# Kernel optimization log

Measured on AMD Instinct MI355X. Metric: run time of the kernel, lower is better.

The kernel has to match this reference:

```python
import jax, jax.numpy as jnp
import numpy as np

B, DIN, DOUT, E, H, K = 8192, 1024, 1024, 8, 128, 2

def setup_inputs() -> dict:
    key = jax.random.key(0)
    ks = jax.random.split(key, 6)
    s = 0.02
    return {
        "x": jax.random.normal(ks[0], (B, DIN), jnp.float32),
        "w1": jax.random.normal(ks[1], (DIN, H), jnp.float32) * s,
        "b1": jnp.zeros((H,), jnp.float32),
        "wg": jax.random.normal(ks[2], (DIN, H), jnp.float32) * s,
        "bg": jnp.zeros((H,), jnp.float32),
        "w2": jax.random.normal(ks[3], (H, E), jnp.float32) * s,
        "b2": jnp.zeros((E,), jnp.float32),
        "we": jax.random.normal(ks[4], (E, DIN, DOUT), jnp.float32) * s,
        "be": jnp.zeros((E, DOUT), jnp.float32),
    }

def reference(x, w1, b1, wg, bg, w2, b2, we, be):
    Bx = x.shape[0]
    Eo = we.shape[0]
    Do = we.shape[2]
    # Router with GLU; NOTE: softmax over BATCH dim (dim=0), as in source.
    h = (x @ w1 + b1) * jax.nn.relu(x @ wg + bg)
    h = jax.nn.relu(h)
    l = jax.nn.softmax(x=(h @ w2 + b2), axis=0)  # [B, E]
    batch_K = -(-K * Bx) // Eo  # ceil(K/E * B), static
    # top-k tokens per expert (along batch dim)
    ws_t, ib_t = jax.lax.top_k(l.T, batch_K)  # [E, bK]
    ws, ib = ws_t.T, ib_t.T                   # [bK, E]
    nws = jax.nn.softmax(ws, axis=0)          # renorm over selected tokens
    # dispatch: gather selected tokens for all experts at once
    sel = x[ib]                                # [bK, E, DIN]
    eo = jnp.einsum('ked,edo->keo', sel, we) + be  # [bK, E, DOUT]
    eo = eo * nws[:, :, None]
    # combine (concat_sum): per-expert scatter-set + shared scatter-add sum
    e_idx = jnp.broadcast_to(jnp.arange(Eo)[None, :], ib.shape)  # [bK, E]
    out_e = jnp.zeros((Eo, Bx, Do), x.dtype).at[e_idx, ib].set(eo)
    temp_sum = jnp.zeros((Bx, Do), x.dtype).at[ib].add(eo)
    out_e = out_e + temp_sum[None]
    return out_e.transpose(1, 0, 2).reshape(Bx, Eo * Do)
```

## Files before the change

kernel.cpp:

```cpp
#include <hip/hip_runtime.h>
#include <math.h>

#define B_TOK 8192
#define D_IN 1024
#define D_OUT 1024
#define N_E 8
#define N_H 128
#define SEL 2048

using bf16x8 = __attribute__((ext_vector_type(8))) short;
using floatx4 = __attribute__((ext_vector_type(4))) float;

__device__ __forceinline__ unsigned short f2bf(float f) {
  unsigned u = __float_as_uint(f);
  u = (u + 0x7FFFu + ((u >> 16) & 1u)) >> 16;
  return (unsigned short)u;
}

__device__ __forceinline__ float bf2f(unsigned short h) {
  return __uint_as_float(((unsigned)h) << 16);
}

__device__ __forceinline__ void async_cp16(const void* g, void* l) {
  __builtin_amdgcn_global_load_lds((__attribute__((address_space(1))) void*)g,
                                   (__attribute__((address_space(3))) void*)l,
                                   16, 0, 0);
}

__global__ __launch_bounds__(256) void k_router_fat(const float* __restrict__ x,
                                                    const float* __restrict__ w1,
                                                    const float* __restrict__ b1,
                                                    const float* __restrict__ wg,
                                                    const float* __restrict__ bg,
                                                    const float* __restrict__ w2,
                                                    const float* __restrict__ b2,
                                                    const float* __restrict__ we,
                                                    unsigned short* __restrict__ xb,
                                                    double* __restrict__ logits,
                                                    unsigned short* __restrict__ web) {
  __shared__ char smem[39168];
  const int t = threadIdx.x;

  if (blockIdx.x >= 512) {
    const int wb = blockIdx.x - 512;
    const int e = wb >> 8;
    const int rem = wb & 255;
    const int o0 = (rem >> 4) * 64;
    const int d0 = (rem & 15) * 64;
    float (*tile)[68] = (float(*)[68])smem;
    const float* wsrc = we + (size_t)e * D_IN * D_OUT;
    unsigned short* wdst = web + (size_t)e * D_OUT * D_IN;
    const int r = t >> 4;
    const int c = (t & 15) * 4;
#pragma unroll
    for (int p = 0; p < 4; ++p) {
      float4 v = *(const float4*)(wsrc + (size_t)(d0 + r + 16 * p) * D_OUT + o0 + c);
      tile[r + 16 * p][c] = v.x; tile[r + 16 * p][c + 1] = v.y;
      tile[r + 16 * p][c + 2] = v.z; tile[r + 16 * p][c + 3] = v.w;
    }
    __syncthreads();
#pragma unroll
    for (int p = 0; p < 4; ++p) {
      int orow = r + 16 * p;
      ushort4 v;
      v.x = f2bf(tile[c + 0][orow]); v.y = f2bf(tile[c + 1][orow]);
      v.z = f2bf(tile[c + 2][orow]); v.w = f2bf(tile[c + 3][orow]);
      *(ushort4*)(wdst + (size_t)(o0 + orow) * D_IN + d0 + c) = v;
    }
    return;
  }

  float (*xs)[36]  = (float(*)[36])(smem);
  float (*ws1)[128] = (float(*)[128])(smem + 2304);
  float (*wsg)[128] = (float(*)[128])(smem + 2304 + 16384);
  float* w2s = (float*)(smem + 2304 + 16384 + 16384);
  const int b0 = blockIdx.x * 16;
  const int tg = t >> 5;
  const int og = t & 31;

  ((float4*)w2s)[t] = ((const float4*)w2)[t];

  double d1[2][4] = {}; double dg[2][4] = {};
  for (int k0 = 0; k0 < D_IN; k0 += 32) {
    __syncthreads();
    if (t < 128) {
      int r = t >> 3, c = (t & 7) * 4;
      float4 v = *(const float4*)(x + (size_t)(b0 + r) * D_IN + k0 + c);
      *(float4*)(&xs[r][c]) = v;
      ushort4 u; u.x = f2bf(v.x); u.y = f2bf(v.y); u.z = f2bf(v.z); u.w = f2bf(v.w);
      *(ushort4*)(xb + (size_t)(b0 + r) * D_IN + k0 + c) = u;
    }
    {
      int r = t >> 5, c = (t & 31) * 4;
#pragma unroll
      for (int p = 0; p < 4; ++p) {
        *(float4*)(&ws1[r + 8 * p][c]) = *(const float4*)(w1 + (size_t)(k0 + r + 8 * p) * N_H + c);
        *(float4*)(&wsg[r + 8 * p][c]) = *(const float4*)(wg + (size_t)(k0 + r + 8 * p) * N_H + c);
      }
    }
    __syncthreads();
    float a1[2][4] = {}; float ag[2][4] = {};
    for (int k = 0; k < 32; k += 4) {
      float xk[2][4];
#pragma unroll
      for (int i = 0; i < 2; ++i) {
        float4 v = *(const float4*)(&xs[tg * 2 + i][k]);
        xk[i][0] = v.x; xk[i][1] = v.y; xk[i][2] = v.z; xk[i][3] = v.w;
      }
#pragma unroll
      for (int kk = 0; kk < 4; ++kk) {
        float4 w1v = *(const float4*)(&ws1[k + kk][og * 4]);
        float4 wgv = *(const float4*)(&wsg[k + kk][og * 4]);
        float wa1[4] = {w1v.x, w1v.y, w1v.z, w1v.w};
        float wag[4] = {wgv.x, wgv.y, wgv.z, wgv.w};
#pragma unroll
        for (int i = 0; i < 2; ++i) {
#pragma unroll
          for (int j = 0; j < 4; ++j) {
            a1[i][j] += xk[i][kk] * wa1[j];
            ag[i][j] += xk[i][kk] * wag[j];
          }
        }
      }
    }
#pragma unroll
    for (int i = 0; i < 2; ++i)
#pragma unroll
      for (int j = 0; j < 4; ++j) { d1[i][j] += a1[i][j]; dg[i][j] += ag[i][j]; }
  }

  float4 b1v = *(const float4*)(b1 + og * 4);
  float4 bgv = *(const float4*)(bg + og * 4);
  float b1a[4] = {b1v.x, b1v.y, b1v.z, b1v.w};
  float bga[4] = {bgv.x, bgv.y, bgv.z, bgv.w};
  float hv[2][4];
#pragma unroll
  for (int i = 0; i < 2; ++i) {
#pragma unroll
    for (int j = 0; j < 4; ++j) {
      float a = (float)d1[i][j] + b1a[j];
      float g = (float)dg[i][j] + bga[j];
      g = fmaxf(g, 0.f);
      hv[i][j] = fmaxf(a * g, 0.f);
    }
  }

  double lp[2][8] = {};
#pragma unroll
  for (int i = 0; i < 2; ++i) {
#pragma unroll
    for (int j = 0; j < 4; ++j) {
      double hj = (double)hv[i][j];
      int kk = og * 4 + j;
#pragma unroll
      for (int e = 0; e < 8; ++e)
        lp[i][e] += hj * (double)w2s[kk * N_E + e];
    }
  }
#pragma unroll
  for (int o = 16; o; o >>= 1) {
#pragma unroll
    for (int i = 0; i < 2; ++i)
#pragma unroll
      for (int e = 0; e < 8; ++e)
        lp[i][e] += __shfl_down(lp[i][e], o);
  }
  if (og == 0) {
#pragma unroll
    for (int i = 0; i < 2; ++i)
#pragma unroll
      for (int e = 0; e < 8; ++e)
        logits[(size_t)(b0 + tg * 2 + i) * N_E + e] = lp[i][e] + (double)b2[e];
  }
}

__global__ __launch_bounds__(256) void k_topk(const double* __restrict__ logits,
                                              int* __restrict__ ib, float* __restrict__ nws,
                                              int* __restrict__ slot) {
  const int e = blockIdx.x;
  const int t = threadIdx.x;
  __shared__ double redd[4];
  __shared__ int redi[4];
  __shared__ unsigned redu[4];
  __shared__ int s_cnt;

  double lv[32];
#pragma unroll
  for (int i = 0; i < 32; ++i) lv[i] = logits[(size_t)(t + i * 256) * N_E + e];

  double m = -1e300;
#pragma unroll
  for (int i = 0; i < 32; ++i) m = fmax(m, lv[i]);
  for (int o = 32; o; o >>= 1) m = fmax(m, __shfl_down(m, o));
  __syncthreads();
  if ((t & 63) == 0) redd[t >> 6] = m;
  __syncthreads();
  const double maxl = fmax(fmax(redd[0], redd[1]), fmax(redd[2], redd[3]));

  double s = 0.0;
#pragma unroll
  for (int i = 0; i < 32; ++i) s += exp(lv[i] - maxl);
  for (int o = 32; o; o >>= 1) s += __shfl_down(s, o);
  __syncthreads();
  if ((t & 63) == 0) redd[t >> 6] = s;
  __syncthreads();
  const double sum = redd[0] + redd[1] + redd[2] + redd[3];

  unsigned kr[32];
#pragma unroll
  for (int i = 0; i < 32; ++i) {
    float lf = (float)(exp(lv[i] - maxl) / sum);
    kr[i] = __float_as_uint(lf);
  }

  unsigned mnk = 0xFFFFFFFFu, mxk = 0;
#pragma unroll
  for (int i = 0; i < 32; ++i) { mnk = (kr[i] < mnk) ? kr[i] : mnk; mxk = (kr[i] > mxk) ? kr[i] : mxk; }
  for (int o = 32; o; o >>= 1) {
    unsigned v = __shfl_down(mnk, o); mnk = (v < mnk) ? v : mnk;
    unsigned w = __shfl_down(mxk, o); mxk = (w > mxk) ? w : mxk;
  }
  __syncthreads();
  if ((t & 63) == 0) redu[t >> 6] = mnk;
  __syncthreads();
  mnk = redu[0]; if (redu[1] < mnk) mnk = redu[1]; if (redu[2] < mnk) mnk = redu[2]; if (redu[3] < mnk) mnk = redu[3];
  __syncthreads();
  if ((t & 63) == 0) redu[t >> 6] = mxk;
  __syncthreads();
  mxk = redu[0]; if (redu[1] > mxk) mxk = redu[1]; if (redu[2] > mxk) mxk = redu[2]; if (redu[3] > mxk) mxk = redu[3];

  const unsigned diff = mnk ^ mxk;
  int hb = -1;
  unsigned thr;
  if (diff == 0) {
    thr = mnk;
  } else {
    hb = 31 - __clz(diff);
    thr = mxk & ~((hb >= 31) ? 0xFFFFFFFFu : ((1u << (hb + 1)) - 1u));
  }

  for (int bit = hb; bit >= 0; --bit) {
    unsigned trial = thr | (1u << bit);
    int c = 0;
#pragma unroll
    for (int i = 0; i < 32; ++i) c += (kr[i] >= trial) ? 1 : 0;
    for (int o = 32; o; o >>= 1) c += __shfl_down(c, o);
    __syncthreads();
    if ((t & 63) == 0) redi[t >> 6] = c;
    __syncthreads();
    c = redi[0] + redi[1] + redi[2] + redi[3];
    if (c >= SEL) thr = trial;
  }

  int c1 = 0, ceq = 0;
#pragma unroll
  for (int i = 0; i < 32; ++i) {
    c1 += (kr[i] > thr) ? 1 : 0;
    ceq += (kr[i] == thr) ? 1 : 0;
  }
  for (int o = 32; o; o >>= 1) { c1 += __shfl_down(c1, o); ceq += __shfl_down(ceq, o); }
  __syncthreads();
  if ((t & 63) == 0) { redi[t >> 6] = c1; ((int*)redu)[t >> 6] = ceq; }
  __syncthreads();
  c1 = redi[0] + redi[1] + redi[2] + redi[3];
  ceq = ((int*)redu)[0] + ((int*)redu)[1] + ((int*)redu)[2] + ((int*)redu)[3];
  const int need = SEL - c1;

  int cut;
  if (ceq == need) {
    cut = B_TOK;
  } else {
    cut = 0;
    for (int bit = 12; bit >= 0; --bit) {
      int trial = cut | (1 << bit);
      int c = 0;
#pragma unroll
      for (int i = 0; i < 32; ++i) c += (kr[i] == thr && (t + i * 256) < trial) ? 1 : 0;
      for (int o = 32; o; o >>= 1) c += __shfl_down(c, o);
      __syncthreads();
      if ((t & 63) == 0) redi[t >> 6] = c;
      __syncthreads();
      c = redi[0] + redi[1] + redi[2] + redi[3];
      if (c < need) cut = trial;
    }
  }

  const double maxw = (double)__uint_as_float(mxk);

  double ss = 0.0;
#pragma unroll
  for (int i = 0; i < 32; ++i) {
    int idx = t + i * 256;
    bool sel = (kr[i] > thr) || (kr[i] == thr && idx <= cut);
    if (sel) ss += exp((double)__uint_as_float(kr[i]) - maxw);
  }
  for (int o = 32; o; o >>= 1) ss += __shfl_down(ss, o);
  __syncthreads();
  if ((t & 63) == 0) redd[t >> 6] = ss;
  __syncthreads();
  const double ssum = redd[0] + redd[1] + redd[2] + redd[3];

  if (t == 0) s_cnt = 0;
#pragma unroll
  for (int i = 0; i < 32; ++i) slot[(size_t)(t + i * 256) * N_E + e] = -1;
  __syncthreads();
  for (int i = 0; i < 32; ++i) {
    int idx = t + i * 256;
    bool sel = (kr[i] > thr) || (kr[i] == thr && idx <= cut);
    if (sel) {
      int pos = atomicAdd(&s_cnt, 1);
      ib[e * SEL + pos] = idx;
      nws[e * SEL + pos] = (float)(exp((double)__uint_as_float(kr[i]) - maxw) / ssum);
      slot[(size_t)idx * N_E + e] = pos;
    }
  }
}

__global__ __launch_bounds__(512, 2) void k_expert_gemm(const unsigned short* __restrict__ xb,
                                                        const unsigned short* __restrict__ web,
                                                        const float* __restrict__ be,
                                                        const int* __restrict__ ib,
                                                        const float* __restrict__ nws,
                                                        unsigned short* __restrict__ eo) {
  __shared__ unsigned short S[2 * 32768];
  __shared__ int rowidx[256];
  __shared__ float nwss[256];
  const int e = blockIdx.z;
  const int bm = blockIdx.x * 256;
  const int bn = blockIdx.y * 256;
  const int t = threadIdx.x;
  const int wave = t >> 6, lane = t & 63;
  if (t < 256) {
    rowidx[t] = ib[e * SEL + bm + t];
    nwss[t] = nws[e * SEL + bm + t];
  }
  __syncthreads();
  const unsigned short* wbase = web + (size_t)e * D_IN * D_OUT;

  const unsigned short* asrc[4];
  const unsigned short* bsrc[4];
  int adst[4], bdst[4];
#pragma unroll
  for (int j = 0; j < 4; ++j) {
    int idx = t + j * 512;
    int r = idx >> 3;
    int c16 = (idx & 7) ^ (r & 7);
    asrc[j] = xb + (size_t)rowidx[r] * D_IN + c16 * 8;
    adst[j] = idx * 8;
    bsrc[j] = wbase + (size_t)(bn + r) * D_IN + c16 * 8;
    bdst[j] = 16384 + idx * 8;
  }

#define STAGE(kt, buf)                                                        \
  {                                                                           \
    _Pragma("unroll")                                                         \
    for (int j = 0; j < 4; ++j) {                                             \
      async_cp16(asrc[j] + (kt) * 64, S + (buf) * 32768 + adst[j]);           \
      async_cp16(bsrc[j] + (kt) * 64, S + (buf) * 32768 + bdst[j]);           \
    }                                                                         \
  }

  floatx4 acc[8][4] = {};
  const int wr = wave >> 2, wc = wave & 3;
  const int fr = lane & 15, fq = lane >> 4;
  const int swz = (fr & 7) << 3;

  STAGE(0, 0);
  STAGE(1, 1);

  for (int kt = 0; kt < 16; ++kt) {
    const int cur = kt & 1;
    if (kt == 15) {
      asm volatile("s_waitcnt vmcnt(0)" ::: "memory");
    } else {
      asm volatile("s_waitcnt vmcnt(8)" ::: "memory");
    }
    __builtin_amdgcn_s_barrier();
    const unsigned short* Ab = S + cur * 32768;
    const unsigned short* Bb = Ab + 16384;
    __builtin_amdgcn_s_setprio(1);
#pragma unroll
    for (int kk = 0; kk < 2; ++kk) {
      bf16x8 af[8], bfr[4];
#pragma unroll
      for (int mt = 0; mt < 8; ++mt)
        af[mt] = *(const bf16x8*)(Ab + (wr * 128 + mt * 16 + fr) * 64 + ((kk * 32 + fq * 8) ^ swz));
#pragma unroll
      for (int nt = 0; nt < 4; ++nt)
        bfr[nt] = *(const bf16x8*)(Bb + (wc * 64 + nt * 16 + fr) * 64 + ((kk * 32 + fq * 8) ^ swz));
#pragma unroll
      for (int mt = 0; mt < 8; ++mt)
#pragma unroll
        for (int nt = 0; nt < 4; ++nt)
          acc[mt][nt] = __builtin_amdgcn_mfma_f32_16x16x32_bf16(af[mt], bfr[nt], acc[mt][nt], 0, 0, 0);
    }
    __builtin_amdgcn_s_setprio(0);
    __builtin_amdgcn_sched_barrier(0);
    __builtin_amdgcn_s_barrier();
    if (kt < 14) STAGE(kt + 2, cur);
  }
#undef STAGE

  float bev[4];
#pragma unroll
  for (int nt = 0; nt < 4; ++nt) bev[nt] = be[e * D_OUT + bn + wc * 64 + nt * 16 + fr];
#pragma unroll
  for (int mt = 0; mt < 8; ++mt) {
#pragma unroll
    for (int r = 0; r < 4; ++r) {
      int lrow = wr * 128 + mt * 16 + fq * 4 + r;
      float nw = nwss[lrow];
      size_t rbase = ((size_t)e * SEL + bm + lrow) * D_OUT;
#pragma unroll
      for (int nt = 0; nt < 4; ++nt) {
        int cc = bn + wc * 64 + nt * 16 + fr;
        eo[rbase + cc] = f2bf((acc[mt][nt][r] + bev[nt]) * nw);
      }
    }
  }
}

__global__ __launch_bounds__(256) void k_combine(const unsigned short* __restrict__ eo,
                                                 const int* __restrict__ slot,
                                                 float* __restrict__ out) {
  const int b = blockIdx.x;
  const int t = threadIdx.x;
  __shared__ int ss[8];
  if (t < 8) ss[t] = slot[(size_t)b * N_E + t];
  __syncthreads();
  const int d0 = t * 4;
  float vx[8], vy[8], vz[8], vw[8];
  float tx = 0.f, ty = 0.f, tz = 0.f, tw = 0.f;
#pragma unroll
  for (int e = 0; e < 8; ++e) {
    int k = ss[e];
    if (k >= 0) {
      ushort4 u = *(const ushort4*)(eo + ((size_t)e * SEL + k) * D_OUT + d0);
      vx[e] = bf2f(u.x); vy[e] = bf2f(u.y); vz[e] = bf2f(u.z); vw[e] = bf2f(u.w);
      tx += vx[e]; ty += vy[e]; tz += vz[e]; tw += vw[e];
    } else {
      vx[e] = 0.f; vy[e] = 0.f; vz[e] = 0.f; vw[e] = 0.f;
    }
  }
#pragma unroll
  for (int e = 0; e < 8; ++e) {
    float4 o;
    o.x = tx + vx[e]; o.y = ty + vy[e]; o.z = tz + vz[e]; o.w = tw + vw[e];
    *(float4*)(out + (size_t)b * (N_E * D_OUT) + e * D_OUT + d0) = o;
  }
}

extern "C" void kernel_launch(void* const* d_in, const int* in_sizes, int n_in,
                              void* d_out, int out_size, void* d_ws, size_t ws_size,
                              hipStream_t stream) {
  const float* x  = (const float*)d_in[0];
  const float* w1 = (const float*)d_in[1];
  const float* b1 = (const float*)d_in[2];
  const float* wg = (const float*)d_in[3];
  const float* bg = (const float*)d_in[4];
  const float* w2 = (const float*)d_in[5];
  const float* b2 = (const float*)d_in[6];
  const float* we = (const float*)d_in[7];
  const float* be = (const float*)d_in[8];
  float* out = (float*)d_out;

  char* ws = (char*)d_ws;
  size_t off = 0;
  auto alloc = [&](size_t bytes) -> void* {
    void* p = ws + off;
    off += (bytes + 255) & ~(size_t)255;
    return p;
  };
  unsigned short* xb  = (unsigned short*)alloc((size_t)B_TOK * D_IN * 2);
  unsigned short* web = (unsigned short*)alloc((size_t)N_E * D_IN * D_OUT * 2);
  unsigned short* eo  = (unsigned short*)alloc((size_t)N_E * SEL * D_OUT * 2);
  double* lgts  = (double*)alloc((size_t)B_TOK * N_E * 8);
  int* ibuf     = (int*)alloc((size_t)N_E * SEL * 4);
  float* nws    = (float*)alloc((size_t)N_E * SEL * 4);
  int* slot     = (int*)alloc((size_t)B_TOK * N_E * 4);
  if (off > ws_size) return;

  hipLaunchKernelGGL(k_router_fat, dim3(512 + 2048), dim3(256), 0, stream,
                     x, w1, b1, wg, bg, w2, b2, we, xb, lgts, web);
  hipLaunchKernelGGL(k_topk, dim3(N_E), dim3(256), 0, stream, lgts, ibuf, nws, slot);
  hipLaunchKernelGGL(k_expert_gemm, dim3(SEL / 256, D_OUT / 256, N_E), dim3(512), 0, stream,
                     xb, web, be, ibuf, nws, eo);
  hipLaunchKernelGGL(k_combine, dim3(B_TOK), dim3(256), 0, stream, eo, slot, out);
}
```

Baseline: 503.5 us.

## Double-buffer router weights with async LDS loads and double tokens per block

The router GEMM now stages w1/wg chunks into a double-buffered LDS region with global_load_lds, prefetching the next chunk and the next x slice while computing the current one. Each block now handles 32 tokens instead of 16, which halves router blocks and the redundant weight reloads across them. Top-k also caches the exp values instead of recomputing them. In exchange, the larger shared memory allocation (about 74KB) lowers occupancy, and the register count rises with the 4x4 double accumulators.

```diff
diff --git a/kernel.cpp b/kernel.cpp
--- a/kernel.cpp
+++ b/kernel.cpp
@@ -38,11 +38,11 @@
                                                     unsigned short* __restrict__ xb,
                                                     double* __restrict__ logits,
                                                     unsigned short* __restrict__ web) {
-  __shared__ char smem[39168];
+  __shared__ __align__(16) char smem[74240];
   const int t = threadIdx.x;
 
-  if (blockIdx.x >= 512) {
-    const int wb = blockIdx.x - 512;
+  if (blockIdx.x >= 256) {
+    const int wb = blockIdx.x - 256;
     const int e = wb >> 8;
     const int rem = wb & 255;
     const int o0 = (rem >> 4) * 64;
@@ -70,51 +70,63 @@
     return;
   }
 
-  float (*xs)[36]  = (float(*)[36])(smem);
-  float (*ws1)[128] = (float(*)[128])(smem + 2304);
-  float (*wsg)[128] = (float(*)[128])(smem + 2304 + 16384);
-  float* w2s = (float*)(smem + 2304 + 16384 + 16384);
-  const int b0 = blockIdx.x * 16;
+  float (*xs)[36] = (float(*)[36])(smem);
+  float* wdbuf = (float*)(smem + 4608);
+  float* w2s = (float*)(smem + 4608 + 65536);
+  const int b0 = blockIdx.x * 32;
   const int tg = t >> 5;
   const int og = t & 31;
+  const int xr = t >> 3, xc = (t & 7) * 4;
 
   ((float4*)w2s)[t] = ((const float4*)w2)[t];
 
-  double d1[2][4] = {}; double dg[2][4] = {};
-  for (int k0 = 0; k0 < D_IN; k0 += 32) {
-    __syncthreads();
-    if (t < 128) {
-      int r = t >> 3, c = (t & 7) * 4;
-      float4 v = *(const float4*)(x + (size_t)(b0 + r) * D_IN + k0 + c);
-      *(float4*)(&xs[r][c]) = v;
+#define STAGEW(ch, buf)                                                       \
+  {                                                                           \
+    _Pragma("unroll")                                                         \
+    for (int j = 0; j < 4; ++j) {                                             \
+      int idx = t + j * 256;                                                  \
+      int rr = idx >> 5, cc = idx & 31;                                       \
+      async_cp16(w1 + (size_t)((ch) * 32 + rr) * N_H + cc * 4,                \
+                 wdbuf + (buf) * 8192 + idx * 4);                             \
+      async_cp16(wg + (size_t)((ch) * 32 + rr) * N_H + cc * 4,                \
+                 wdbuf + (buf) * 8192 + 4096 + idx * 4);                      \
+    }                                                                         \
+  }
+
+  STAGEW(0, 0);
+  float4 v = *(const float4*)(x + (size_t)(b0 + xr) * D_IN + xc);
+
+  double d1[4][4] = {}; double dg[4][4] = {};
+  for (int ch = 0; ch < 32; ++ch) {
+    const int cur = ch & 1;
+    *(float4*)(&xs[xr][xc]) = v;
+    {
       ushort4 u; u.x = f2bf(v.x); u.y = f2bf(v.y); u.z = f2bf(v.z); u.w = f2bf(v.w);
-      *(ushort4*)(xb + (size_t)(b0 + r) * D_IN + k0 + c) = u;
-    }
-    {
-      int r = t >> 5, c = (t & 31) * 4;
-#pragma unroll
-      for (int p = 0; p < 4; ++p) {
-        *(float4*)(&ws1[r + 8 * p][c]) = *(const float4*)(w1 + (size_t)(k0 + r + 8 * p) * N_H + c);
-        *(float4*)(&wsg[r + 8 * p][c]) = *(const float4*)(wg + (size_t)(k0 + r + 8 * p) * N_H + c);
+      *(ushort4*)(xb + (size_t)(b0 + xr) * D_IN + ch * 32 + xc) = u;
+    }
+    asm volatile("s_waitcnt vmcnt(0) lgkmcnt(0)" ::: "memory");
+    __builtin_amdgcn_s_barrier();
+    if (ch < 31) {
+      STAGEW(ch + 1, cur ^ 1);
+      v = *(const float4*)(x + (size_t)(b0 + xr) * D_IN + (ch + 1) * 32 + xc);
+    }
+    const float* wd = wdbuf + cur * 8192;
+    float a1[4][4] = {}; float ag[4][4] = {};
+    for (int k = 0; k < 32; k += 4) {
+      float xk[4][4];
+#pragma unroll
+      for (int i = 0; i < 4; ++i) {
+        float4 xv = *(const float4*)(&xs[tg * 4 + i][k]);
+        xk[i][0] = xv.x; xk[i][1] = xv.y; xk[i][2] = xv.z; xk[i][3] = xv.w;
       }
-    }
-    __syncthreads();
-    float a1[2][4] = {}; float ag[2][4] = {};
-    for (int k = 0; k < 32; k += 4) {
-      float xk[2][4];
-#pragma unroll
-      for (int i = 0; i < 2; ++i) {
-        float4 v = *(const float4*)(&xs[tg * 2 + i][k]);
-        xk[i][0] = v.x; xk[i][1] = v.y; xk[i][2] = v.z; xk[i][3] = v.w;
-      }
 #pragma unroll
       for (int kk = 0; kk < 4; ++kk) {
-        float4 w1v = *(const float4*)(&ws1[k + kk][og * 4]);
-        float4 wgv = *(const float4*)(&wsg[k + kk][og * 4]);
+        float4 w1v = *(const float4*)(wd + (k + kk) * N_H + og * 4);
+        float4 wgv = *(const float4*)(wd + 4096 + (k + kk) * N_H + og * 4);
         float wa1[4] = {w1v.x, w1v.y, w1v.z, w1v.w};
         float wag[4] = {wgv.x, wgv.y, wgv.z, wgv.w};
 #pragma unroll
-        for (int i = 0; i < 2; ++i) {
+        for (int i = 0; i < 4; ++i) {
 #pragma unroll
           for (int j = 0; j < 4; ++j) {
             a1[i][j] += xk[i][kk] * wa1[j];
@@ -124,18 +136,20 @@
       }
     }
 #pragma unroll
-    for (int i = 0; i < 2; ++i)
+    for (int i = 0; i < 4; ++i)
 #pragma unroll
       for (int j = 0; j < 4; ++j) { d1[i][j] += a1[i][j]; dg[i][j] += ag[i][j]; }
-  }
+    __builtin_amdgcn_s_barrier();
+  }
+#undef STAGEW
 
   float4 b1v = *(const float4*)(b1 + og * 4);
   float4 bgv = *(const float4*)(bg + og * 4);
   float b1a[4] = {b1v.x, b1v.y, b1v.z, b1v.w};
   float bga[4] = {bgv.x, bgv.y, bgv.z, bgv.w};
-  float hv[2][4];
-#pragma unroll
-  for (int i = 0; i < 2; ++i) {
+  float hv[4][4];
+#pragma unroll
+  for (int i = 0; i < 4; ++i) {
 #pragma unroll
     for (int j = 0; j < 4; ++j) {
       float a = (float)d1[i][j] + b1a[j];
@@ -145,9 +159,9 @@
     }
   }
 
-  double lp[2][8] = {};
-#pragma unroll
-  for (int i = 0; i < 2; ++i) {
+  double lp[4][8] = {};
+#pragma unroll
+  for (int i = 0; i < 4; ++i) {
 #pragma unroll
     for (int j = 0; j < 4; ++j) {
       double hj = (double)hv[i][j];
@@ -160,17 +174,17 @@
 #pragma unroll
   for (int o = 16; o; o >>= 1) {
 #pragma unroll
-    for (int i = 0; i < 2; ++i)
+    for (int i = 0; i < 4; ++i)
 #pragma unroll
       for (int e = 0; e < 8; ++e)
         lp[i][e] += __shfl_down(lp[i][e], o);
   }
   if (og == 0) {
 #pragma unroll
-    for (int i = 0; i < 2; ++i)
+    for (int i = 0; i < 4; ++i)
 #pragma unroll
       for (int e = 0; e < 8; ++e)
-        logits[(size_t)(b0 + tg * 2 + i) * N_E + e] = lp[i][e] + (double)b2[e];
+        logits[(size_t)(b0 + tg * 4 + i) * N_E + e] = lp[i][e] + (double)b2[e];
   }
 }
 
@@ -197,9 +211,13 @@
   __syncthreads();
   const double maxl = fmax(fmax(redd[0], redd[1]), fmax(redd[2], redd[3]));
 
+  double ev[32];
+#pragma unroll
+  for (int i = 0; i < 32; ++i) ev[i] = exp(lv[i] - maxl);
+
   double s = 0.0;
 #pragma unroll
-  for (int i = 0; i < 32; ++i) s += exp(lv[i] - maxl);
+  for (int i = 0; i < 32; ++i) s += ev[i];
   for (int o = 32; o; o >>= 1) s += __shfl_down(s, o);
   __syncthreads();
   if ((t & 63) == 0) redd[t >> 6] = s;
@@ -209,7 +227,7 @@
   unsigned kr[32];
 #pragma unroll
   for (int i = 0; i < 32; ++i) {
-    float lf = (float)(exp(lv[i] - maxl) / sum);
+    float lf = (float)(ev[i] / sum);
     kr[i] = __float_as_uint(lf);
   }
 
@@ -480,7 +498,7 @@
   int* slot     = (int*)alloc((size_t)B_TOK * N_E * 4);
   if (off > ws_size) return;
 
-  hipLaunchKernelGGL(k_router_fat, dim3(512 + 2048), dim3(256), 0, stream,
+  hipLaunchKernelGGL(k_router_fat, dim3(256 + 2048), dim3(256), 0, stream,
                      x, w1, b1, wg, bg, w2, b2, we, xb, lgts, web);
   hipLaunchKernelGGL(k_topk, dim3(N_E), dim3(256), 0, stream, lgts, ibuf, nws, slot);
   hipLaunchKernelGGL(k_expert_gemm, dim3(SEL / 256, D_OUT / 256, N_E), dim3(512), 0, stream,
```

After: 508.7 us. About the same (+1.0%).
